# Performance work log

Hardware: AMD Instinct MI355X
Metric: run time of the kernel (lower is better)

The kernel has to match this reference:

```python
import jax, jax.numpy as jnp
import numpy as np

TOP_K = 10
RANKING_WEIGHT = 0.3
UP_WEIGHT = 1.0
DOWN_WEIGHT = 0.5
NEG = 1e9  # finite stand-in for -inf so softmax/grads stay NaN-free


def setup_inputs() -> dict:
    key = jax.random.key(0)
    k1, k2, k3, k4 = jax.random.split(key, 4)
    B, N = 1024, 5000
    up_logits = jax.random.normal(k1, (B, N), jnp.float32)
    down_logits = jax.random.normal(k2, (B, N), jnp.float32)
    y_true = jax.random.normal(k3, (B, N), jnp.float32) * 0.05  # daily returns
    masks = jax.random.randint(k4, (B, N), 0, 2).astype(jnp.int32)
    return {"up_logits": up_logits, "down_logits": down_logits,
            "y_true": y_true, "masks": masks}


def _bce_with_logits(x, z):
    # softplus(x) - x*z  ==  -[z*log(sig(x)) + (1-z)*log(1-sig(x))]
    return jax.nn.softplus(x) - x * z


def reference(up_logits, down_logits, y_true, masks):
    maskb = masks > 0                                   # [B, N]
    maskf = maskb.astype(up_logits.dtype)
    num_valid = maskf.sum(-1)                           # [B]
    nv_safe = jnp.maximum(num_valid, 1.0)
    k = jnp.minimum(TOP_K, num_valid.astype(jnp.int32))  # [B] min(top_k, num)

    # Descending rank of y_true among valid entries (invalid pushed to bottom).
    y_desc = jnp.where(maskb, y_true, -NEG)
    rank_desc = jnp.argsort(jnp.argsort(-y_desc, axis=-1), axis=-1)  # [B, N]
    up_labels = (rank_desc < k[:, None]).astype(up_logits.dtype)

    # Ascending rank (biggest losers) for down path.
    y_asc = jnp.where(maskb, y_true, NEG)
    rank_asc = jnp.argsort(jnp.argsort(y_asc, axis=-1), axis=-1)
    down_labels = (rank_asc < k[:, None]).astype(down_logits.dtype)

    # Mean BCE over valid entries per row.
    up_loss = jnp.sum(_bce_with_logits(up_logits, up_labels) * maskf, -1) / nv_safe
    down_loss = jnp.sum(_bce_with_logits(down_logits, down_labels) * maskf, -1) / nv_safe

    # Listwise KL: softmax over valid entries; kl_div(log p, q, 'batchmean')
    # with 1D input of size num divides the sum by num.
    logp = jax.nn.log_softmax(jnp.where(maskb, up_logits, -NEG), axis=-1)
    logq = jax.nn.log_softmax(jnp.where(maskb, y_true, -NEG), axis=-1)
    q = jnp.exp(logq)
    kl = jnp.sum(jnp.where(maskb, q * (logq - logp), 0.0), -1) / nv_safe

    batch_loss = UP_WEIGHT * up_loss + DOWN_WEIGHT * down_loss + RANKING_WEIGHT * kl
    batch_loss = jnp.where(num_valid > 0, batch_loss, 0.0)  # skip empty rows
    return jnp.sum(batch_loss) / up_logits.shape[0]
```

## Files before the change

### kernel.cpp

```cpp
#include <hip/hip_runtime.h>
#include <math.h>

#define NCOLS 5000
#define NF4   1250
#define BLOCK 256
#define NWAVES (BLOCK / 64)
#define NITER 5
#define TOPKK 10
#define TR    3
#define CAP 128

__device__ __forceinline__ unsigned mono_f32(float f) {
  unsigned u = __float_as_uint(f);
  return (u & 0x80000000u) ? ~u : (u | 0x80000000u);
}

__device__ __forceinline__ float wave_sum_f(float v) {
#pragma unroll
  for (int o = 1; o < 64; o <<= 1) v += __shfl_xor(v, o);
  return v;
}
__device__ __forceinline__ int wave_sum_i(int v) {
#pragma unroll
  for (int o = 1; o < 64; o <<= 1) v += __shfl_xor(v, o);
  return v;
}
__device__ __forceinline__ unsigned wave_max_u(unsigned v) {
#pragma unroll
  for (int o = 1; o < 64; o <<= 1) {
    unsigned w = __shfl_xor(v, o);
    v = w > v ? w : v;
  }
  return v;
}

extern "C" __global__ __launch_bounds__(BLOCK, 4)
void row_loss_kernel(const float* __restrict__ up, const float* __restrict__ down,
                     const float* __restrict__ yt, const int* __restrict__ masks,
                     float* __restrict__ out, float inv_nrows) {
  __shared__ uint4 km_s[NITER * BLOCK];
  __shared__ float red_f[6][NWAVES];
  __shared__ int red_i[NWAVES];
  __shared__ unsigned t1w_t[NWAVES];
  __shared__ unsigned t1w_b[NWAVES];
  __shared__ unsigned keys_t[CAP];
  __shared__ int      col_t[CAP];
  __shared__ unsigned keys_b[CAP];
  __shared__ int      col_b[CAP];
  __shared__ int ct, cb;
  __shared__ float s_res[2];

  const int tid = threadIdx.x;
  const int lane = tid & 63;
  const int wv = tid >> 6;
  const int row = blockIdx.x;
  const long long b4 = (long long)row * NF4;
  const long long base = (long long)row * NCOLS;

  const float4* up4 = (const float4*)up + b4;
  const float4* dn4 = (const float4*)down + b4;
  const float4* yt4 = (const float4*)yt + b4;
  const int4*   mk4 = (const int4*)masks + b4;

  if (tid == 0) { ct = 0; cb = 0; }

  float4 y4[NITER], u4[NITER], d4[NITER];
  int4 m4[NITER];
#pragma unroll
  for (int j = 0; j < NITER; ++j) {
    const int f = j * BLOCK + tid;
    const int fc = f < NF4 ? f : NF4 - 1;
    y4[j] = yt4[fc];
    u4[j] = up4[fc];
    d4[j] = dn4[fc];
    m4[j] = mk4[fc];
  }
  __builtin_amdgcn_sched_barrier(0);

  int nv_l = 0;
  float sq = 0.f, sp = 0.f, seyy = 0.f, seyu = 0.f, aspu = 0.f, aspd = 0.f;
  unsigned tmax = 0u, tbmax = 0u;
#pragma unroll
  for (int j = 0; j < NITER; ++j) {
    const bool inb = (j * BLOCK + tid) < NF4;
    const float* yp = (const float*)&y4[j];
    const float* upp = (const float*)&u4[j];
    const float* dp = (const float*)&d4[j];
    const int* mp = (const int*)&m4[j];
    unsigned kk[4];
#pragma unroll
    for (int c = 0; c < 4; ++c) {
      const bool valid = inb && (mp[c] > 0);
      const float y = yp[c], u = upp[c], d = dp[c];
      const unsigned kd = valid ? mono_f32(y) : 0u;
      const unsigned kb = valid ? ~kd : 0u;
      kk[c] = kd;
      tmax = kd > tmax ? kd : tmax;
      tbmax = kb > tbmax ? kb : tbmax;
      if (valid) {
        nv_l++;
        const float ey = __expf(y);
        const float eu = __expf(u);
        const float ed = __expf(d);
        sq += ey;
        seyy += ey * y;
        seyu += ey * u;
        sp += eu;
        aspu += (u > 15.f) ? u : __logf(1.f + eu);
        aspd += (d > 15.f) ? d : __logf(1.f + ed);
      }
    }
    km_s[j * BLOCK + tid] = make_uint4(kk[0], kk[1], kk[2], kk[3]);
  }

  nv_l = wave_sum_i(nv_l);
  sq = wave_sum_f(sq);
  sp = wave_sum_f(sp);
  seyy = wave_sum_f(seyy);
  seyu = wave_sum_f(seyu);
  aspu = wave_sum_f(aspu);
  aspd = wave_sum_f(aspd);
  if (lane == 0) {
    red_i[wv] = nv_l;
    red_f[0][wv] = sq;  red_f[1][wv] = sp;
    red_f[2][wv] = seyy; red_f[3][wv] = seyu;
    red_f[4][wv] = aspu; red_f[5][wv] = aspd;
  }

  {
    unsigned vt = tmax, vb = tbmax, t1t = 0u, t1b = 0u;
#pragma unroll
    for (int r = 0; r < TR; ++r) {
      unsigned mt = wave_max_u(vt);
      unsigned mb = wave_max_u(vb);
      if (vt == mt) vt = 0u;
      if (vb == mb) vb = 0u;
      t1t = mt; t1b = mb;
    }
    if (lane == 0) { t1w_t[wv] = t1t; t1w_b[wv] = t1b; }
  }
  __syncthreads();

  int nv = 0;
#pragma unroll
  for (int w = 0; w < NWAVES; ++w) nv += red_i[w];
  const int k = nv < TOPKK ? nv : TOPKK;

  unsigned t1 = 0xFFFFFFFFu, t1b = 0xFFFFFFFFu;
#pragma unroll
  for (int w = 0; w < NWAVES; ++w) {
    t1 = t1w_t[w] < t1 ? t1w_t[w] : t1;
    t1b = t1w_b[w] < t1b ? t1w_b[w] : t1b;
  }

#pragma unroll
  for (int j = 0; j < NITER; ++j) {
    const uint4 kk4 = km_s[j * BLOCK + tid];
    const unsigned ka[4] = {kk4.x, kk4.y, kk4.z, kk4.w};
#pragma unroll
    for (int c = 0; c < 4; ++c) {
      const unsigned kd = ka[c];
      if (kd != 0u) {
        const int col = ((j * BLOCK + tid) << 2) + c;
        if (kd >= t1) {
          int i = atomicAdd(&ct, 1);
          if (i < CAP) { keys_t[i] = kd; col_t[i] = col; }
        }
        const unsigned kb = ~kd;
        if (kb >= t1b) {
          int i = atomicAdd(&cb, 1);
          if (i < CAP) { keys_b[i] = kb; col_b[i] = col; }
        }
      }
    }
  }
  __syncthreads();

  if (wv == 0) {
    const int n = ct < CAP ? ct : CAP;
    const unsigned k0 = (lane < n) ? keys_t[lane] : 0u;
    const unsigned k1 = (64 + lane < n) ? keys_t[64 + lane] : 0u;
    unsigned thr = 0u;
#pragma unroll
    for (int b = 31; b >= 0; --b) {
      const unsigned t = thr | (1u << b);
      const int c = __popcll(__ballot(k0 >= t)) + __popcll(__ballot(k1 >= t));
      thr = (c >= k) ? t : thr;
    }
    float su = 0.f;
    if (k0 >= thr && k0 != 0u) su += up[base + col_t[lane]];
    if (k1 >= thr && k1 != 0u) su += up[base + col_t[64 + lane]];
    su = wave_sum_f(su);
    if (lane == 0) s_res[0] = su;
  } else if (wv == 1) {
    const int n = cb < CAP ? cb : CAP;
    const unsigned k0 = (lane < n) ? keys_b[lane] : 0u;
    const unsigned k1 = (64 + lane < n) ? keys_b[64 + lane] : 0u;
    unsigned thr = 0u;
#pragma unroll
    for (int b = 31; b >= 0; --b) {
      const unsigned t = thr | (1u << b);
      const int c = __popcll(__ballot(k0 >= t)) + __popcll(__ballot(k1 >= t));
      thr = (c >= k) ? t : thr;
    }
    float sd = 0.f;
    if (k0 >= thr && k0 != 0u) sd += down[base + col_b[lane]];
    if (k1 >= thr && k1 != 0u) sd += down[base + col_b[64 + lane]];
    sd = wave_sum_f(sd);
    if (lane == 0) s_res[1] = sd;
  }
  __syncthreads();

  if (tid == 0 && nv > 0) {
    float SQ = 0.f, SP = 0.f, SYY = 0.f, SYU = 0.f, ASU = 0.f, ASD = 0.f;
#pragma unroll
    for (int w = 0; w < NWAVES; ++w) {
      SQ += red_f[0][w]; SP += red_f[1][w];
      SYY += red_f[2][w]; SYU += red_f[3][w];
      ASU += red_f[4][w]; ASD += red_f[5][w];
    }
    const float SU = s_res[0];
    const float SD = s_res[1];
    const float kl = (SYY - SYU) / SQ - __logf(SQ) + __logf(SP);
    const float up_loss = ASU - SU;
    const float dn_loss = ASD - SD;
    const float loss = (up_loss + 0.5f * dn_loss + 0.3f * kl) / (float)nv;
    atomicAdd(out, loss * inv_nrows);
  }
}

extern "C" void kernel_launch(void* const* d_in, const int* in_sizes, int n_in,
                              void* d_out, int out_size, void* d_ws, size_t ws_size,
                              hipStream_t stream) {
  const float* up_logits   = (const float*)d_in[0];
  const float* down_logits = (const float*)d_in[1];
  const float* y_true      = (const float*)d_in[2];
  const int*   masks       = (const int*)d_in[3];

  const int nrows = in_sizes[0] / NCOLS;

  hipMemsetAsync(d_out, 0, sizeof(float) * (size_t)out_size, stream);
  row_loss_kernel<<<nrows, BLOCK, 0, stream>>>(up_logits, down_logits, y_true,
                                               masks, (float*)d_out,
                                               1.0f / (float)nrows);
}
```

Baseline: 116.5 us.

## Split each row across four blocks with a second kernel merging top-k candidates

Splits every row into four column quarters handled by separate blocks. Each block computes its partial sums and a per-quarter candidate set of top and bottom keys, storing the logit values with them. A new finish kernel gives one wave per row, merges the partials, runs the radix threshold over the 256 candidates and accumulates the loss. This raises the number of blocks and removes the shared-memory key staging and the gathers from global memory. The cost is a second kernel launch plus workspace traffic, and each quarter keeps at most 64 candidates per direction, which is assumed to be enough.

```diff
diff --git a/kernel.cpp b/kernel.cpp
--- a/kernel.cpp
+++ b/kernel.cpp
@@ -3,12 +3,14 @@
 
 #define NCOLS 5000
 #define NF4   1250
+#define QBLK  4
+#define QF4   313
 #define BLOCK 256
 #define NWAVES (BLOCK / 64)
-#define NITER 5
 #define TOPKK 10
 #define TR    3
-#define CAP 128
+#define CAP   64
+
 
 __device__ __forceinline__ unsigned mono_f32(float f) {
   unsigned u = __float_as_uint(f);
@@ -34,84 +36,81 @@
   return v;
 }
 
-extern "C" __global__ __launch_bounds__(BLOCK, 4)
-void row_loss_kernel(const float* __restrict__ up, const float* __restrict__ down,
-                     const float* __restrict__ yt, const int* __restrict__ masks,
-                     float* __restrict__ out, float inv_nrows) {
-  __shared__ uint4 km_s[NITER * BLOCK];
-  __shared__ float red_f[6][NWAVES];
-  __shared__ int red_i[NWAVES];
-  __shared__ unsigned t1w_t[NWAVES];
-  __shared__ unsigned t1w_b[NWAVES];
-  __shared__ unsigned keys_t[CAP];
-  __shared__ int      col_t[CAP];
-  __shared__ unsigned keys_b[CAP];
-  __shared__ int      col_b[CAP];
+extern "C" __global__ __launch_bounds__(BLOCK, 6)
+void part_kernel(const float* __restrict__ up, const float* __restrict__ down,
+                 const float* __restrict__ yt, const int* __restrict__ masks,
+                 float* __restrict__ ws_sums, float2* __restrict__ ws_top,
+                 float2* __restrict__ ws_bot) {
+  __shared__ float red_f[7][NWAVES];
+  __shared__ unsigned t1w_t[NWAVES], t1w_b[NWAVES];
+  __shared__ unsigned keys_t[CAP]; __shared__ float vals_t[CAP];
+  __shared__ unsigned keys_b[CAP]; __shared__ float vals_b[CAP];
   __shared__ int ct, cb;
-  __shared__ float s_res[2];
 
   const int tid = threadIdx.x;
   const int lane = tid & 63;
   const int wv = tid >> 6;
-  const int row = blockIdx.x;
-  const long long b4 = (long long)row * NF4;
-  const long long base = (long long)row * NCOLS;
+  const int bq = blockIdx.x;
+  const int row = bq >> 2;
+  const int q = bq & 3;
+  const int s = q * QF4;
+  const int e = (s + QF4) < NF4 ? (s + QF4) : NF4;
+  const int cnt = e - s;
+  const long long b4 = (long long)row * NF4 + s;
+
+  if (tid == 0) { ct = 0; cb = 0; }
+  if (tid < CAP) {
+    keys_t[tid] = 0u; vals_t[tid] = 0.f;
+    keys_b[tid] = 0u; vals_b[tid] = 0.f;
+  }
 
   const float4* up4 = (const float4*)up + b4;
   const float4* dn4 = (const float4*)down + b4;
   const float4* yt4 = (const float4*)yt + b4;
   const int4*   mk4 = (const int4*)masks + b4;
 
-  if (tid == 0) { ct = 0; cb = 0; }
-
-  float4 y4[NITER], u4[NITER], d4[NITER];
-  int4 m4[NITER];
-#pragma unroll
-  for (int j = 0; j < NITER; ++j) {
-    const int f = j * BLOCK + tid;
-    const int fc = f < NF4 ? f : NF4 - 1;
-    y4[j] = yt4[fc];
-    u4[j] = up4[fc];
-    d4[j] = dn4[fc];
-    m4[j] = mk4[fc];
-  }
+  const int t2 = BLOCK + tid;
+  const bool inb2 = t2 < cnt;
+  const int f2 = inb2 ? t2 : cnt - 1;
+  float4 y0 = yt4[tid], u0 = up4[tid], d0 = dn4[tid];
+  float4 y1 = yt4[f2],  u1 = up4[f2],  d1 = dn4[f2];
+  int4   m0 = mk4[tid], m1 = mk4[f2];
   __builtin_amdgcn_sched_barrier(0);
 
   int nv_l = 0;
   float sq = 0.f, sp = 0.f, seyy = 0.f, seyu = 0.f, aspu = 0.f, aspd = 0.f;
+  unsigned kk[8]; float ua[8], da[8];
   unsigned tmax = 0u, tbmax = 0u;
-#pragma unroll
-  for (int j = 0; j < NITER; ++j) {
-    const bool inb = (j * BLOCK + tid) < NF4;
-    const float* yp = (const float*)&y4[j];
-    const float* upp = (const float*)&u4[j];
-    const float* dp = (const float*)&d4[j];
-    const int* mp = (const int*)&m4[j];
-    unsigned kk[4];
-#pragma unroll
-    for (int c = 0; c < 4; ++c) {
-      const bool valid = inb && (mp[c] > 0);
-      const float y = yp[c], u = upp[c], d = dp[c];
-      const unsigned kd = valid ? mono_f32(y) : 0u;
-      const unsigned kb = valid ? ~kd : 0u;
-      kk[c] = kd;
-      tmax = kd > tmax ? kd : tmax;
-      tbmax = kb > tbmax ? kb : tbmax;
-      if (valid) {
-        nv_l++;
-        const float ey = __expf(y);
-        const float eu = __expf(u);
-        const float ed = __expf(d);
-        sq += ey;
-        seyy += ey * y;
-        seyu += ey * u;
-        sp += eu;
-        aspu += (u > 15.f) ? u : __logf(1.f + eu);
-        aspd += (d > 15.f) ? d : __logf(1.f + ed);
-      }
-    }
-    km_s[j * BLOCK + tid] = make_uint4(kk[0], kk[1], kk[2], kk[3]);
-  }
+
+#define ELEM(idx, Y, U, D, M, INB)                                      \
+  {                                                                     \
+    const bool valid = (INB) && ((M) > 0);                              \
+    const float y = (Y), u = (U), d = (D);                              \
+    const unsigned kd = valid ? mono_f32(y) : 0u;                       \
+    const unsigned kb = valid ? ~kd : 0u;                               \
+    kk[idx] = kd; ua[idx] = u; da[idx] = d;                             \
+    tmax = kd > tmax ? kd : tmax;                                       \
+    tbmax = kb > tbmax ? kb : tbmax;                                    \
+    if (valid) {                                                        \
+      nv_l++;                                                           \
+      const float ey = __expf(y);                                       \
+      const float eu = __expf(u);                                       \
+      const float ed = __expf(d);                                       \
+      sq += ey; seyy += ey * y; seyu += ey * u; sp += eu;               \
+      aspu += (u > 15.f) ? u : __logf(1.f + eu);                        \
+      aspd += (d > 15.f) ? d : __logf(1.f + ed);                        \
+    }                                                                   \
+  }
+
+  ELEM(0, y0.x, u0.x, d0.x, m0.x, true)
+  ELEM(1, y0.y, u0.y, d0.y, m0.y, true)
+  ELEM(2, y0.z, u0.z, d0.z, m0.z, true)
+  ELEM(3, y0.w, u0.w, d0.w, m0.w, true)
+  ELEM(4, y1.x, u1.x, d1.x, m1.x, inb2)
+  ELEM(5, y1.y, u1.y, d1.y, m1.y, inb2)
+  ELEM(6, y1.z, u1.z, d1.z, m1.z, inb2)
+  ELEM(7, y1.w, u1.w, d1.w, m1.w, inb2)
+#undef ELEM
 
   nv_l = wave_sum_i(nv_l);
   sq = wave_sum_f(sq);
@@ -121,10 +120,10 @@
   aspu = wave_sum_f(aspu);
   aspd = wave_sum_f(aspd);
   if (lane == 0) {
-    red_i[wv] = nv_l;
-    red_f[0][wv] = sq;  red_f[1][wv] = sp;
-    red_f[2][wv] = seyy; red_f[3][wv] = seyu;
-    red_f[4][wv] = aspu; red_f[5][wv] = aspd;
+    red_f[0][wv] = (float)nv_l;
+    red_f[1][wv] = sq;  red_f[2][wv] = sp;
+    red_f[3][wv] = seyy; red_f[4][wv] = seyu;
+    red_f[5][wv] = aspu; red_f[6][wv] = aspd;
   }
 
   {
@@ -141,91 +140,106 @@
   }
   __syncthreads();
 
-  int nv = 0;
-#pragma unroll
-  for (int w = 0; w < NWAVES; ++w) nv += red_i[w];
-  const int k = nv < TOPKK ? nv : TOPKK;
-
-  unsigned t1 = 0xFFFFFFFFu, t1b = 0xFFFFFFFFu;
+  unsigned tq_t = 0xFFFFFFFFu, tq_b = 0xFFFFFFFFu;
 #pragma unroll
   for (int w = 0; w < NWAVES; ++w) {
-    t1 = t1w_t[w] < t1 ? t1w_t[w] : t1;
-    t1b = t1w_b[w] < t1b ? t1w_b[w] : t1b;
-  }
-
-#pragma unroll
-  for (int j = 0; j < NITER; ++j) {
-    const uint4 kk4 = km_s[j * BLOCK + tid];
-    const unsigned ka[4] = {kk4.x, kk4.y, kk4.z, kk4.w};
-#pragma unroll
-    for (int c = 0; c < 4; ++c) {
-      const unsigned kd = ka[c];
-      if (kd != 0u) {
-        const int col = ((j * BLOCK + tid) << 2) + c;
-        if (kd >= t1) {
-          int i = atomicAdd(&ct, 1);
-          if (i < CAP) { keys_t[i] = kd; col_t[i] = col; }
+    tq_t = t1w_t[w] < tq_t ? t1w_t[w] : tq_t;
+    tq_b = t1w_b[w] < tq_b ? t1w_b[w] : tq_b;
+  }
+
+  if (tid < 7) {
+    float sm = red_f[tid][0] + red_f[tid][1] + red_f[tid][2] + red_f[tid][3];
+    ws_sums[bq * 8 + tid] = sm;
+  }
+
+#pragma unroll
+  for (int i = 0; i < 8; ++i) {
+    const unsigned kd = kk[i];
+    if (kd != 0u) {
+      if (kd >= tq_t) {
+        int p = atomicAdd(&ct, 1);
+        if (p < CAP) { keys_t[p] = kd; vals_t[p] = ua[i]; }
+      }
+      const unsigned kb = ~kd;
+      if (kb >= tq_b) {
+        int p = atomicAdd(&cb, 1);
+        if (p < CAP) { keys_b[p] = kb; vals_b[p] = da[i]; }
+      }
+    }
+  }
+  __syncthreads();
+
+  if (tid < CAP) {
+    ws_top[bq * CAP + tid] = make_float2(__uint_as_float(keys_t[tid]), vals_t[tid]);
+  } else if (tid < 2 * CAP) {
+    const int i = tid - CAP;
+    ws_bot[bq * CAP + i] = make_float2(__uint_as_float(keys_b[i]), vals_b[i]);
+  }
+}
+
+extern "C" __global__ __launch_bounds__(256, 4)
+void finish_kernel(const float* __restrict__ ws_sums,
+                   const float2* __restrict__ ws_top,
+                   const float2* __restrict__ ws_bot,
+                   float* __restrict__ out, int nrows, float inv_nrows) {
+  __shared__ float wl[NWAVES];
+  const int tid = threadIdx.x;
+  const int lane = tid & 63;
+  const int wv = tid >> 6;
+  const int row = blockIdx.x * NWAVES + wv;
+
+  float loss = 0.f;
+  if (row < nrows) {
+    float v = 0.f;
+    if (lane < 32) v = ws_sums[(row * QBLK + (lane >> 3)) * 8 + (lane & 7)];
+    v += __shfl_xor(v, 8);
+    v += __shfl_xor(v, 16);
+    const float nvf = __shfl(v, 0);
+    const int nv = (int)nvf;
+    if (nv > 0) {
+      const int k = nv < TOPKK ? nv : TOPKK;
+      const int cb0 = row * QBLK * CAP;
+      unsigned kt[4], kb[4]; float vt[4], vb[4];
+#pragma unroll
+      for (int t = 0; t < 4; ++t) {
+        const float2 a = ws_top[cb0 + t * 64 + lane];
+        const float2 b = ws_bot[cb0 + t * 64 + lane];
+        kt[t] = __float_as_uint(a.x); vt[t] = a.y;
+        kb[t] = __float_as_uint(b.x); vb[t] = b.y;
+      }
+      unsigned thr_t = 0u, thr_b = 0u;
+#pragma unroll
+      for (int b = 31; b >= 0; --b) {
+        const unsigned tt = thr_t | (1u << b);
+        const unsigned tb = thr_b | (1u << b);
+        int c1 = 0, c2 = 0;
+#pragma unroll
+        for (int t = 0; t < 4; ++t) {
+          c1 += __popcll(__ballot(kt[t] >= tt));
+          c2 += __popcll(__ballot(kb[t] >= tb));
         }
-        const unsigned kb = ~kd;
-        if (kb >= t1b) {
-          int i = atomicAdd(&cb, 1);
-          if (i < CAP) { keys_b[i] = kb; col_b[i] = col; }
-        }
-      }
+        thr_t = (c1 >= k) ? tt : thr_t;
+        thr_b = (c2 >= k) ? tb : thr_b;
+      }
+      float su = 0.f, sd = 0.f;
+#pragma unroll
+      for (int t = 0; t < 4; ++t) {
+        if (kt[t] >= thr_t && kt[t] != 0u) su += vt[t];
+        if (kb[t] >= thr_b && kb[t] != 0u) sd += vb[t];
+      }
+      su = wave_sum_f(su);
+      sd = wave_sum_f(sd);
+      const float SQ  = __shfl(v, 1), SP  = __shfl(v, 2);
+      const float SYY = __shfl(v, 3), SYU = __shfl(v, 4);
+      const float ASU = __shfl(v, 5), ASD = __shfl(v, 6);
+      const float kl = (SYY - SYU) / SQ - __logf(SQ) + __logf(SP);
+      loss = ((ASU - su) + 0.5f * (ASD - sd) + 0.3f * kl) / nvf;
     }
   }
+  if (lane == 0) wl[wv] = loss;
   __syncthreads();
-
-  if (wv == 0) {
-    const int n = ct < CAP ? ct : CAP;
-    const unsigned k0 = (lane < n) ? keys_t[lane] : 0u;
-    const unsigned k1 = (64 + lane < n) ? keys_t[64 + lane] : 0u;
-    unsigned thr = 0u;
-#pragma unroll
-    for (int b = 31; b >= 0; --b) {
-      const unsigned t = thr | (1u << b);
-      const int c = __popcll(__ballot(k0 >= t)) + __popcll(__ballot(k1 >= t));
-      thr = (c >= k) ? t : thr;
-    }
-    float su = 0.f;
-    if (k0 >= thr && k0 != 0u) su += up[base + col_t[lane]];
-    if (k1 >= thr && k1 != 0u) su += up[base + col_t[64 + lane]];
-    su = wave_sum_f(su);
-    if (lane == 0) s_res[0] = su;
-  } else if (wv == 1) {
-    const int n = cb < CAP ? cb : CAP;
-    const unsigned k0 = (lane < n) ? keys_b[lane] : 0u;
-    const unsigned k1 = (64 + lane < n) ? keys_b[64 + lane] : 0u;
-    unsigned thr = 0u;
-#pragma unroll
-    for (int b = 31; b >= 0; --b) {
-      const unsigned t = thr | (1u << b);
-      const int c = __popcll(__ballot(k0 >= t)) + __popcll(__ballot(k1 >= t));
-      thr = (c >= k) ? t : thr;
-    }
-    float sd = 0.f;
-    if (k0 >= thr && k0 != 0u) sd += down[base + col_b[lane]];
-    if (k1 >= thr && k1 != 0u) sd += down[base + col_b[64 + lane]];
-    sd = wave_sum_f(sd);
-    if (lane == 0) s_res[1] = sd;
-  }
-  __syncthreads();
-
-  if (tid == 0 && nv > 0) {
-    float SQ = 0.f, SP = 0.f, SYY = 0.f, SYU = 0.f, ASU = 0.f, ASD = 0.f;
-#pragma unroll
-    for (int w = 0; w < NWAVES; ++w) {
-      SQ += red_f[0][w]; SP += red_f[1][w];
-      SYY += red_f[2][w]; SYU += red_f[3][w];
-      ASU += red_f[4][w]; ASD += red_f[5][w];
-    }
-    const float SU = s_res[0];
-    const float SD = s_res[1];
-    const float kl = (SYY - SYU) / SQ - __logf(SQ) + __logf(SP);
-    const float up_loss = ASU - SU;
-    const float dn_loss = ASD - SD;
-    const float loss = (up_loss + 0.5f * dn_loss + 0.3f * kl) / (float)nv;
-    atomicAdd(out, loss * inv_nrows);
+  if (tid == 0) {
+    atomicAdd(out, (wl[0] + wl[1] + wl[2] + wl[3]) * inv_nrows);
   }
 }
 
@@ -238,9 +252,21 @@
   const int*   masks       = (const int*)d_in[3];
 
   const int nrows = in_sizes[0] / NCOLS;
+  const int nrq = nrows * QBLK;
+  const size_t need = (size_t)nrq * (8 + 4 * CAP) * sizeof(float);
 
   hipMemsetAsync(d_out, 0, sizeof(float) * (size_t)out_size, stream);
-  row_loss_kernel<<<nrows, BLOCK, 0, stream>>>(up_logits, down_logits, y_true,
-                                               masks, (float*)d_out,
-                                               1.0f / (float)nrows);
-}
+
+  float* wsf = (float*)d_ws;
+  float* ws_sums = wsf;
+  float2* ws_top = (float2*)(wsf + (size_t)nrq * 8);
+  float2* ws_bot = ws_top + (size_t)nrq * CAP;
+  (void)need; (void)ws_size;
+
+  part_kernel<<<nrq, BLOCK, 0, stream>>>(up_logits, down_logits, y_true, masks,
+                                         ws_sums, ws_top, ws_bot);
+  const int p2blocks = (nrows + NWAVES - 1) / NWAVES;
+  finish_kernel<<<p2blocks, 256, 0, stream>>>(ws_sums, ws_top, ws_bot,
+                                              (float*)d_out, nrows,
+                                              1.0f / (float)nrows);
+}
```

Measured after the change: 124.8 us. 7.1% more time.
